# Kernel tuning notes

Hardware: AMD Instinct MI355X
Metric: run time of the kernel (lower is better)

## Reference

```python
import jax, jax.numpy as jnp
import numpy as np

B, S, H = 16, 1024, 768


def setup_inputs() -> dict:
    key = jax.random.key(0)
    ks = jax.random.split(key, 12)
    s = 1.0 / np.sqrt(H)
    return {
        "encoder_outputs": jax.random.normal(ks[0], (B, S, H), dtype=jnp.float32),
        "mask": jax.random.randint(ks[1], (B, S), 0, 2, dtype=jnp.int32),
        "Wq": jax.random.uniform(ks[2], (H, H), jnp.float32, -s, s),
        "bq": jnp.zeros((H,), jnp.float32),
        "Wk": jax.random.uniform(ks[3], (H, H), jnp.float32, -s, s),
        "bk": jnp.zeros((H,), jnp.float32),
        "Wv": jax.random.uniform(ks[4], (H, H), jnp.float32, -s, s),
        "bv": jnp.zeros((H,), jnp.float32),
        "W1": jax.random.uniform(ks[5], (H, H), jnp.float32, -s, s),
        "b1": jnp.zeros((H,), jnp.float32),
        "W2": jax.random.uniform(ks[6], (H, H), jnp.float32, -s, s),
        "b2": jnp.zeros((H,), jnp.float32),
    }


def reference(encoder_outputs, mask, Wq, bq, Wk, bk, Wv, bv, W1, b1, W2, b2):
    x = encoder_outputs  # [B, S, H]
    inv_sqrt_h = 1.0 / jnp.sqrt(jnp.asarray(H, x.dtype))
    # ReLU-gated query/key projections (dropout=0 -> identity)
    q = jax.nn.relu(jnp.einsum('bsh,oh->bso', x, Wq) + bq)
    k = jax.nn.relu(jnp.einsum('bsh,oh->bso', x, Wk) + bk)
    score = jnp.einsum('bsh,bth->bst', q, k) * inv_sqrt_h  # [B, S, S]
    v = jnp.einsum('bsh,oh->bso', x, Wv) + bv
    m = mask.astype(x.dtype)  # [B, S]
    new_mask = m[:, :, None] * m[:, None, :]  # outer product [B, S, S]
    score = score - (1.0 - new_mask) * 1e12
    w = jax.nn.softmax(score, axis=2) * new_mask
    out = jnp.einsum('bst,bth->bsh', w, v)
    # FFN residual
    h1 = jax.nn.relu(jnp.einsum('bsh,oh->bso', out, W1) + b1)
    out = jnp.einsum('bsh,oh->bso', h1, W2) + b2 + out
    return out
```

## Files before the change

### kernel.cpp

```cpp
#include <hip/hip_runtime.h>
#include <hip/hip_bf16.h>

typedef __bf16 bf16_t;
typedef __bf16 bf16x8 __attribute__((ext_vector_type(8)));
typedef __bf16 bf16x4 __attribute__((ext_vector_type(4)));
typedef float f32x4 __attribute__((ext_vector_type(4)));
typedef unsigned int u32;
typedef const __attribute__((address_space(1))) u32* gptr_t;
typedef __attribute__((address_space(3))) u32* lptr_t;

static constexpr int Bb = 16, Ss = 1024, Hh = 768;

__global__ __launch_bounds__(256) void compact_mask(
    const int* __restrict__ mask, int* __restrict__ tok, int* __restrict__ cnt)
{
    const int b = blockIdx.x;
    const int t = threadIdx.x;
    const int4 m4 = *(const int4*)&mask[(b << 10) + (t << 2)];
    const int c = (m4.x != 0) + (m4.y != 0) + (m4.z != 0) + (m4.w != 0);
    __shared__ int sb[256];
    sb[t] = c;
    __syncthreads();
    for (int off = 1; off < 256; off <<= 1) {
        int v = (t >= off) ? sb[t - off] : 0;
        __syncthreads();
        sb[t] += v;
        __syncthreads();
    }
    int p = sb[t] - c;
    int* tb = tok + (b << 10);
    if (m4.x) tb[p++] = (t << 2) + 0;
    if (m4.y) tb[p++] = (t << 2) + 1;
    if (m4.z) tb[p++] = (t << 2) + 2;
    if (m4.w) tb[p++] = (t << 2) + 3;
    if (t == 255) cnt[b] = sb[255];
}

__global__ __launch_bounds__(256) void cvt_all(
    const float* __restrict__ x,
    const float* __restrict__ w0, const float* __restrict__ w1,
    const float* __restrict__ w2, const float* __restrict__ w3,
    const float* __restrict__ w4,
    const float* __restrict__ bq, const float* __restrict__ bk,
    const float* __restrict__ bv,
    const float* __restrict__ b1, const float* __restrict__ b2,
    const int* __restrict__ tok, const int* __restrict__ cnt,
    bf16_t* __restrict__ xc, bf16_t* __restrict__ wdst, float* __restrict__ bdst,
    float* __restrict__ cvec)
{
    const int bx = blockIdx.x;
    const int t = threadIdx.x;
    if (bx < 2880) {
        int seg = bx / 576;
        const float* src = seg == 0 ? w0 : seg == 1 ? w1 : seg == 2 ? w2 : seg == 3 ? w3 : w4;
        int i = (bx % 576) * 256 + t;
        float4 v = ((const float4*)src)[i];
        bf16x4 o = { (bf16_t)v.x, (bf16_t)v.y, (bf16_t)v.z, (bf16_t)v.w };
        ((bf16x4*)(wdst + (long)seg * 589824))[i] = o;
    } else if (bx < 2889) {
        int i = (bx - 2880) * 256 + t;
        if (i < 2304)
            bdst[i] = i < 768 ? bq[i] : i < 1536 ? bk[i - 768] : bv[i - 1536];
    } else if (bx < 19273) {
        const int idx = bx - 2889;
        const int b = idx >> 10, j = idx & 1023;
        if (j < cnt[b] && t < 192) {
            const int s = tok[(b << 10) + j];
            float4 v = ((const float4*)(x + ((long)((b << 10) + s)) * 768))[t];
            bf16x4 o = { (bf16_t)v.x, (bf16_t)v.y, (bf16_t)v.z, (bf16_t)v.w };
            ((bf16x4*)(xc + ((long)((b << 10) + j)) * 768))[t] = o;
        }
    } else {
        const int o = ((bx - 19273) << 3) + (t >> 5);
        const int l = t & 31;
        const float* wr = w4 + (long)o * 768;
        float acc = 0.f;
        for (int h = l; h < 768; h += 32) acc += wr[h] * fmaxf(b1[h], 0.f);
#pragma unroll
        for (int off = 16; off; off >>= 1) acc += __shfl_down(acc, off, 32);
        if (l == 0) cvec[o] = acc + b2[o];
    }
}

__device__ __forceinline__ void async_cp16(const void* g, void* l)
{
    __builtin_amdgcn_global_load_lds((gptr_t)g, (lptr_t)l, 16, 0, 0);
}

enum { EG_QKV = 0, EG_SCORE_C = 1, EG_PV = 2, EG_FFN1 = 3, EG_FFN2 = 4 };

#define SBAR __builtin_amdgcn_s_barrier()
#define VMW(n) asm volatile("s_waitcnt vmcnt(" #n ")" ::: "memory")

template <int EPI, int NT>
__global__ __launch_bounds__(512) void mfma_gemm(
    const bf16_t* __restrict__ A, const bf16_t* __restrict__ B,
    const float* __restrict__ bias, const bf16_t* __restrict__ resid,
    const int* __restrict__ tok, const int* __restrict__ cnt,
    void* __restrict__ Cout, bf16_t* __restrict__ out2, bf16_t* __restrict__ out3,
    int K, int lda, int ldb, long sA, long sB, float scale)
{
    int tot = 0;
#pragma unroll
    for (int b = 0; b < 16; b++) {
        int a = (cnt[b] + 127) >> 7;
        tot += (EPI == EG_SCORE_C) ? a * a : a * NT;
    }
    const int raw = blockIdx.x;
    if (raw >= tot) return;
    const int q = tot >> 3, r = tot & 7;
    const int xcd = raw & 7, pos = raw >> 3;
    int v = xcd * q + (xcd < r ? xcd : r) + pos;
    int bz = 0;
    for (;;) {
        int a = (cnt[bz] + 127) >> 7;
        int t = (EPI == EG_SCORE_C) ? a * a : a * NT;
        if (v < t) break;
        v -= t; ++bz;
    }
    int mi, ni;
    if constexpr (EPI == EG_SCORE_C) {
        int a = (cnt[bz] + 127) >> 7;
        mi = v / a; ni = v - mi * a;
    } else {
        mi = v / NT; ni = v - mi * NT;
    }
    const int cb = cnt[bz];
    const int m0 = mi << 7;
    const int n0 = ni << 7;
    const int Kend = (EPI == EG_PV) ? ((cb + 63) & ~63) : K;
    const int nk = Kend >> 6;

    constexpr int MI = 2, NI = 4;
    constexpr int TSZ = 128 * 64;

    __shared__ __align__(16) bf16_t Asl[2 * TSZ];
    __shared__ __align__(16) bf16_t Bsl[2 * TSZ];

    const int tid = threadIdx.x;
    const int wid = tid >> 6;
    const int lane = tid & 63;
    const int wm = wid & 3, wn = wid >> 2;

    const bf16_t* Ab = A + (long)bz * sA;
    const bf16_t* Bp = B + (long)bz * sB;

    const int srow8 = lane >> 3;
    const int scg = ((lane & 7) ^ srow8) << 3;

    const bf16_t* pa[2];
    const bf16_t* pb[2];
#pragma unroll
    for (int qq = 0; qq < 2; qq++) {
        pa[qq] = Ab + (long)(m0 + (wid << 4) + (qq << 3) + srow8) * lda + scg;
        pb[qq] = Bp + (long)(n0 + (wid << 4) + (qq << 3) + srow8) * ldb + scg;
    }
    const int wrow = wid << 4;

    const int arow = lane & 15;
    const int axr = lane & 7;
    const int f0 = (arow << 6) + (((lane >> 4)      ^ axr) << 3);
    const int f1 = (arow << 6) + ((((lane >> 4) + 4) ^ axr) << 3);

    auto stage = [&](int tk, int buf) {
        const long ko = (long)tk << 6;
#pragma unroll
        for (int qq = 0; qq < 2; qq++) {
            async_cp16(pa[qq] + ko, &Asl[buf * TSZ + ((wrow + (qq << 3)) << 6)]);
            async_cp16(pb[qq] + ko, &Bsl[buf * TSZ + ((wrow + (qq << 3)) << 6)]);
        }
    };

    f32x4 acc[MI][NI] = {};

    stage(0, 0);
    __builtin_amdgcn_sched_barrier(0);
    VMW(0); SBAR;

    for (int t = 0; t < nk; ++t) {
        if (t + 1 < nk) stage(t + 1, (t + 1) & 1);

        const int cba = (t & 1) * TSZ;
        bf16x8 af[MI][2], bfr[NI][2];
#pragma unroll
        for (int i = 0; i < MI; i++) {
            const int rb = cba + ((wm * MI + i) << 10);
            af[i][0] = *(const bf16x8*)&Asl[rb + f0];
            af[i][1] = *(const bf16x8*)&Asl[rb + f1];
        }
#pragma unroll
        for (int j = 0; j < NI; j++) {
            const int rb = cba + ((wn * NI + j) << 10);
            bfr[j][0] = *(const bf16x8*)&Bsl[rb + f0];
            bfr[j][1] = *(const bf16x8*)&Bsl[rb + f1];
        }
        __builtin_amdgcn_sched_barrier(0);
#pragma unroll
        for (int kk = 0; kk < 2; kk++)
#pragma unroll
            for (int i = 0; i < MI; i++)
#pragma unroll
                for (int j = 0; j < NI; j++)
                    acc[i][j] = __builtin_amdgcn_mfma_f32_16x16x32_bf16(
                        af[i][kk], bfr[j][kk], acc[i][j], 0, 0, 0);
        __builtin_amdgcn_sched_barrier(0);
        if (t + 1 < nk) { VMW(0); SBAR; }
    }

    const int mb_ = m0 + wm * 32;
    const int nb_ = n0 + wn * 64;
    const int colw = lane & 15;
    const int rowq = (lane >> 4) << 2;

    if constexpr (EPI == EG_QKV) {
        float bj[NI];
#pragma unroll
        for (int j = 0; j < NI; j++) bj[j] = bias[nb_ + (j << 4) + colw];
        if (nb_ < 1536) {
            bf16_t* C = ((nb_ < 768) ? (bf16_t*)Cout : out2) + (long)bz * 786432;
            const int cbase = (nb_ < 768) ? nb_ : nb_ - 768;
#pragma unroll
            for (int i = 0; i < MI; i++)
#pragma unroll
                for (int j = 0; j < NI; j++)
#pragma unroll
                    for (int r2 = 0; r2 < 4; r2++) {
                        int row = mb_ + (i << 4) + rowq + r2;
                        int col = cbase + (j << 4) + colw;
                        C[(long)row * Hh + col] = (bf16_t)fmaxf(acc[i][j][r2] + bj[j], 0.f);
                    }
        } else {
            bf16_t* C = out3 + (long)bz * 786432;
#pragma unroll
            for (int i = 0; i < MI; i++) {
                const int jc0 = mb_ + (i << 4) + rowq;
#pragma unroll
                for (int j = 0; j < NI; j++) {
                    const int col = nb_ - 1536 + (j << 4) + colw;
                    bf16x4 o = { (bf16_t)(acc[i][j][0] + bj[j]), (bf16_t)(acc[i][j][1] + bj[j]),
                                 (bf16_t)(acc[i][j][2] + bj[j]), (bf16_t)(acc[i][j][3] + bj[j]) };
                    *(bf16x4*)&C[(long)col * 1024 + jc0] = o;
                }
            }
        }
    } else if constexpr (EPI == EG_SCORE_C) {
        bf16_t* C = (bf16_t*)Cout + (long)bz * 1048576;
#pragma unroll
        for (int i = 0; i < MI; i++) {
            const int kbase = mb_ + (i << 4) + rowq;
#pragma unroll
            for (int j = 0; j < NI; j++) {
                const int qrow = nb_ + (j << 4) + colw;
                bf16x4 o = { (bf16_t)(acc[i][j][0] * scale), (bf16_t)(acc[i][j][1] * scale),
                             (bf16_t)(acc[i][j][2] * scale), (bf16_t)(acc[i][j][3] * scale) };
                *(bf16x4*)&C[(long)qrow * 1024 + kbase] = o;
            }
        }
    } else if constexpr (EPI == EG_FFN2) {
        float* outp = (float*)Cout;
        const bf16_t* crow = resid + (long)bz * 786432;
        const int* tb = tok + (bz << 10);
        float bj[NI];
#pragma unroll
        for (int j = 0; j < NI; j++) bj[j] = bias[nb_ + (j << 4) + colw];
#pragma unroll
        for (int i = 0; i < MI; i++)
#pragma unroll
            for (int r2 = 0; r2 < 4; r2++) {
                const int jq = mb_ + (i << 4) + rowq + r2;
                if (jq < cb) {
                    const int s = tb[jq];
                    float* orow = outp + ((long)((bz << 10) + s)) * 768;
                    const bf16_t* cr = crow + (long)jq * 768;
#pragma unroll
                    for (int j = 0; j < NI; j++) {
                        const int col = nb_ + (j << 4) + colw;
                        orow[col] = acc[i][j][r2] + bj[j] + (float)cr[col];
                    }
                }
            }
    } else {
        bf16_t* C = (bf16_t*)Cout + (long)bz * 786432;
        float bj[NI];
#pragma unroll
        for (int j = 0; j < NI; j++) bj[j] = 0.f;
        if constexpr (EPI == EG_FFN1) {
#pragma unroll
            for (int j = 0; j < NI; j++) bj[j] = bias[nb_ + (j << 4) + colw];
        }
#pragma unroll
        for (int i = 0; i < MI; i++)
#pragma unroll
            for (int j = 0; j < NI; j++)
#pragma unroll
                for (int r2 = 0; r2 < 4; r2++) {
                    int row = mb_ + (i << 4) + rowq + r2;
                    int col = nb_ + (j << 4) + colw;
                    float val = acc[i][j][r2] + bj[j];
                    if constexpr (EPI == EG_FFN1) val = fmaxf(val, 0.f);
                    C[(long)row * Hh + col] = (bf16_t)val;
                }
    }
}

__global__ __launch_bounds__(256) void softmax_rows(
    bf16_t* __restrict__ S_, const int* __restrict__ cnt,
    const int* __restrict__ mask, const float* __restrict__ cvec,
    float* __restrict__ out)
{
    const int b = blockIdx.y;
    const int t = threadIdx.x;

    if (blockIdx.z == 1) {
        const int s = blockIdx.x;
        if (t >= 192 || mask[(b << 10) + s]) return;
        float4 v = ((const float4*)cvec)[t];
        ((float4*)(out + ((long)((b << 10) + s)) * 768))[t] = v;
        return;
    }

    const int jq = blockIdx.x;
    const int cb = cnt[b];
    if (jq >= cb) return;
    bf16_t* p = S_ + (((long)(b << 10)) + jq) * 1024;
    const int t0 = t << 2;

    bf16x4 v4 = *(const bf16x4*)&p[t0];
    float v0 = (t0 + 0 < cb) ? (float)v4[0] : -1e30f;
    float v1 = (t0 + 1 < cb) ? (float)v4[1] : -1e30f;
    float v2 = (t0 + 2 < cb) ? (float)v4[2] : -1e30f;
    float v3 = (t0 + 3 < cb) ? (float)v4[3] : -1e30f;

    float mx = fmaxf(fmaxf(v0, v1), fmaxf(v2, v3));
#pragma unroll
    for (int off = 32; off; off >>= 1) mx = fmaxf(mx, __shfl_down(mx, off, 64));
    __shared__ float redm[4], reds[4];
    if ((t & 63) == 0) redm[t >> 6] = mx;
    __syncthreads();
    mx = fmaxf(fmaxf(redm[0], redm[1]), fmaxf(redm[2], redm[3]));

    float e0 = __expf(v0 - mx), e1 = __expf(v1 - mx);
    float e2 = __expf(v2 - mx), e3 = __expf(v3 - mx);
    float sm = e0 + e1 + e2 + e3;
#pragma unroll
    for (int off = 32; off; off >>= 1) sm += __shfl_down(sm, off, 64);
    if ((t & 63) == 0) reds[t >> 6] = sm;
    __syncthreads();
    sm = reds[0] + reds[1] + reds[2] + reds[3];

    const float inv = 1.f / sm;
    bf16x4 o = { (bf16_t)(e0 * inv), (bf16_t)(e1 * inv),
                 (bf16_t)(e2 * inv), (bf16_t)(e3 * inv) };
    *(bf16x4*)&p[t0] = o;
}

extern "C" void kernel_launch(void* const* d_in, const int* in_sizes, int n_in,
                              void* d_out, int out_size, void* d_ws, size_t ws_size,
                              hipStream_t stream)
{
    const float* x  = (const float*)d_in[0];
    const int* mask = (const int*)d_in[1];
    const float* Wq = (const float*)d_in[2];
    const float* bq = (const float*)d_in[3];
    const float* Wk = (const float*)d_in[4];
    const float* bk = (const float*)d_in[5];
    const float* Wv = (const float*)d_in[6];
    const float* bv = (const float*)d_in[7];
    const float* W1 = (const float*)d_in[8];
    const float* b1 = (const float*)d_in[9];
    const float* W2 = (const float*)d_in[10];
    const float* b2 = (const float*)d_in[11];
    float* out = (float*)d_out;

    char* w = (char*)d_ws;
    bf16_t* xc   = (bf16_t*)(w + 0);
    bf16_t* qc   = (bf16_t*)(w + 25165824);
    bf16_t* kc   = (bf16_t*)(w + 50331648);
    bf16_t* vTc  = (bf16_t*)(w + 75497472);
    bf16_t* sc   = (bf16_t*)(w + 100663296);
    bf16_t* wqkv = (bf16_t*)(w + 134217728);
    bf16_t* w1b  = (bf16_t*)(w + 137756672);
    bf16_t* w2b  = (bf16_t*)(w + 138936320);
    float*  bqkv = (float*) (w + 140115968);
    int*    tok  = (int*)   (w + 140125184);
    int*    cnt  = (int*)   (w + 140190720);
    float*  cvec = (float*) (w + 140190784);
    bf16_t* ctxc = xc;
    bf16_t* h1c  = qc;

    const float inv_sqrt_h = 0.036084391824351615f;
    dim3 blk(256);
    dim3 blk8(512);

    compact_mask<<<16, blk, 0, stream>>>(mask, tok, cnt);
    cvt_all<<<19369, blk, 0, stream>>>(x, Wq, Wk, Wv, W1, W2, bq, bk, bv, b1, b2,
                                       tok, cnt, xc, wqkv, bqkv, cvec);

    mfma_gemm<EG_QKV, 18><<<2304, blk8, 0, stream>>>(
        xc, wqkv, bqkv, nullptr, tok, cnt, qc, kc, vTc,
        768, 768, 768, 786432, 0, 1.f);

    mfma_gemm<EG_SCORE_C, 1><<<1024, blk8, 0, stream>>>(
        kc, qc, nullptr, nullptr, tok, cnt, sc, nullptr, nullptr,
        768, 768, 768, 786432, 786432, inv_sqrt_h);

    softmax_rows<<<dim3(1024, 16, 2), blk, 0, stream>>>(sc, cnt, mask, cvec, out);

    mfma_gemm<EG_PV, 6><<<768, blk8, 0, stream>>>(
        sc, vTc, nullptr, nullptr, tok, cnt, ctxc, nullptr, nullptr,
        0, 1024, 1024, 1048576, 786432, 1.f);

    mfma_gemm<EG_FFN1, 6><<<768, blk8, 0, stream>>>(
        ctxc, w1b, b1, nullptr, tok, cnt, h1c, nullptr, nullptr,
        768, 768, 768, 786432, 0, 1.f);

    mfma_gemm<EG_FFN2, 6><<<768, blk8, 0, stream>>>(
        h1c, w2b, b2, ctxc, tok, cnt, out, nullptr, nullptr,
        768, 768, 768, 786432, 0, 1.f);
}
```

Before: 269.5 us.

## Fuse GEMM and softmax stages into one persistent cooperative kernel with grid syncs

Replaces the five separate GEMM launches and the softmax launch with a single cooperative persistent kernel. The kernel loops over tiles per phase and separates phases with grid.sync(). The softmax is rewritten so that one wavefront handles one row, reducing with xor shuffles and no LDS barriers. The goal is to remove launch gaps and tail effects between stages. The cost is that grid-wide barriers are imposed, the XCD-aware tile remapping is dropped, and the grid size is capped by occupancy, which may reduce parallelism for the large QKV phase.

Result: slower. 534.6 us (+98.3%).

```diff
diff --git a/kernel.cpp b/kernel.cpp
--- a/kernel.cpp
+++ b/kernel.cpp
@@ -1,5 +1,8 @@
 #include <hip/hip_runtime.h>
 #include <hip/hip_bf16.h>
+#include <hip/hip_cooperative_groups.h>
+
+namespace cg = cooperative_groups;
 
 typedef __bf16 bf16_t;
 typedef __bf16 bf16x8 __attribute__((ext_vector_type(8)));
@@ -92,8 +95,11 @@
 #define SBAR __builtin_amdgcn_s_barrier()
 #define VMW(n) asm volatile("s_waitcnt vmcnt(" #n ")" ::: "memory")
 
+static constexpr int TSZ = 128 * 64;
+
 template <int EPI, int NT>
-__global__ __launch_bounds__(512) void mfma_gemm(
+__device__ void gemm_phase(
+    bf16_t* Asl, bf16_t* Bsl,
     const bf16_t* __restrict__ A, const bf16_t* __restrict__ B,
     const float* __restrict__ bias, const bf16_t* __restrict__ resid,
     const int* __restrict__ tok, const int* __restrict__ cnt,
@@ -106,119 +112,178 @@
         int a = (cnt[b] + 127) >> 7;
         tot += (EPI == EG_SCORE_C) ? a * a : a * NT;
     }
-    const int raw = blockIdx.x;
-    if (raw >= tot) return;
-    const int q = tot >> 3, r = tot & 7;
-    const int xcd = raw & 7, pos = raw >> 3;
-    int v = xcd * q + (xcd < r ? xcd : r) + pos;
-    int bz = 0;
-    for (;;) {
-        int a = (cnt[bz] + 127) >> 7;
-        int t = (EPI == EG_SCORE_C) ? a * a : a * NT;
-        if (v < t) break;
-        v -= t; ++bz;
-    }
-    int mi, ni;
-    if constexpr (EPI == EG_SCORE_C) {
-        int a = (cnt[bz] + 127) >> 7;
-        mi = v / a; ni = v - mi * a;
-    } else {
-        mi = v / NT; ni = v - mi * NT;
-    }
-    const int cb = cnt[bz];
-    const int m0 = mi << 7;
-    const int n0 = ni << 7;
-    const int Kend = (EPI == EG_PV) ? ((cb + 63) & ~63) : K;
-    const int nk = Kend >> 6;
 
     constexpr int MI = 2, NI = 4;
-    constexpr int TSZ = 128 * 64;
-
-    __shared__ __align__(16) bf16_t Asl[2 * TSZ];
-    __shared__ __align__(16) bf16_t Bsl[2 * TSZ];
-
     const int tid = threadIdx.x;
     const int wid = tid >> 6;
     const int lane = tid & 63;
     const int wm = wid & 3, wn = wid >> 2;
-
-    const bf16_t* Ab = A + (long)bz * sA;
-    const bf16_t* Bp = B + (long)bz * sB;
-
     const int srow8 = lane >> 3;
     const int scg = ((lane & 7) ^ srow8) << 3;
-
-    const bf16_t* pa[2];
-    const bf16_t* pb[2];
-#pragma unroll
-    for (int qq = 0; qq < 2; qq++) {
-        pa[qq] = Ab + (long)(m0 + (wid << 4) + (qq << 3) + srow8) * lda + scg;
-        pb[qq] = Bp + (long)(n0 + (wid << 4) + (qq << 3) + srow8) * ldb + scg;
-    }
     const int wrow = wid << 4;
-
     const int arow = lane & 15;
     const int axr = lane & 7;
     const int f0 = (arow << 6) + (((lane >> 4)      ^ axr) << 3);
     const int f1 = (arow << 6) + ((((lane >> 4) + 4) ^ axr) << 3);
-
-    auto stage = [&](int tk, int buf) {
-        const long ko = (long)tk << 6;
-#pragma unroll
-        for (int qq = 0; qq < 2; qq++) {
-            async_cp16(pa[qq] + ko, &Asl[buf * TSZ + ((wrow + (qq << 3)) << 6)]);
-            async_cp16(pb[qq] + ko, &Bsl[buf * TSZ + ((wrow + (qq << 3)) << 6)]);
-        }
-    };
-
-    f32x4 acc[MI][NI] = {};
-
-    stage(0, 0);
-    __builtin_amdgcn_sched_barrier(0);
-    VMW(0); SBAR;
-
-    for (int t = 0; t < nk; ++t) {
-        if (t + 1 < nk) stage(t + 1, (t + 1) & 1);
-
-        const int cba = (t & 1) * TSZ;
-        bf16x8 af[MI][2], bfr[NI][2];
-#pragma unroll
-        for (int i = 0; i < MI; i++) {
-            const int rb = cba + ((wm * MI + i) << 10);
-            af[i][0] = *(const bf16x8*)&Asl[rb + f0];
-            af[i][1] = *(const bf16x8*)&Asl[rb + f1];
-        }
-#pragma unroll
-        for (int j = 0; j < NI; j++) {
-            const int rb = cba + ((wn * NI + j) << 10);
-            bfr[j][0] = *(const bf16x8*)&Bsl[rb + f0];
-            bfr[j][1] = *(const bf16x8*)&Bsl[rb + f1];
-        }
-        __builtin_amdgcn_sched_barrier(0);
-#pragma unroll
-        for (int kk = 0; kk < 2; kk++)
-#pragma unroll
-            for (int i = 0; i < MI; i++)
-#pragma unroll
-                for (int j = 0; j < NI; j++)
-                    acc[i][j] = __builtin_amdgcn_mfma_f32_16x16x32_bf16(
-                        af[i][kk], bfr[j][kk], acc[i][j], 0, 0, 0);
-        __builtin_amdgcn_sched_barrier(0);
-        if (t + 1 < nk) { VMW(0); SBAR; }
-    }
-
-    const int mb_ = m0 + wm * 32;
-    const int nb_ = n0 + wn * 64;
     const int colw = lane & 15;
     const int rowq = (lane >> 4) << 2;
 
-    if constexpr (EPI == EG_QKV) {
-        float bj[NI];
-#pragma unroll
-        for (int j = 0; j < NI; j++) bj[j] = bias[nb_ + (j << 4) + colw];
-        if (nb_ < 1536) {
-            bf16_t* C = ((nb_ < 768) ? (bf16_t*)Cout : out2) + (long)bz * 786432;
-            const int cbase = (nb_ < 768) ? nb_ : nb_ - 768;
+    for (int w = blockIdx.x; w < tot; w += gridDim.x) {
+        int wv = w, bz = 0;
+        for (;;) {
+            int a = (cnt[bz] + 127) >> 7;
+            int t = (EPI == EG_SCORE_C) ? a * a : a * NT;
+            if (wv < t) break;
+            wv -= t; ++bz;
+        }
+        int mi, ni;
+        if constexpr (EPI == EG_SCORE_C) {
+            int a = (cnt[bz] + 127) >> 7;
+            mi = wv / a; ni = wv - mi * a;
+        } else {
+            mi = wv / NT; ni = wv - mi * NT;
+        }
+        const int cb = cnt[bz];
+        const int m0 = mi << 7;
+        const int n0 = ni << 7;
+        const int Kend = (EPI == EG_PV) ? ((cb + 63) & ~63) : K;
+        const int nk = Kend >> 6;
+
+        const bf16_t* Ab = A + (long)bz * sA;
+        const bf16_t* Bp = B + (long)bz * sB;
+        const bf16_t* pa[2];
+        const bf16_t* pb[2];
+#pragma unroll
+        for (int qq = 0; qq < 2; qq++) {
+            pa[qq] = Ab + (long)(m0 + (wid << 4) + (qq << 3) + srow8) * lda + scg;
+            pb[qq] = Bp + (long)(n0 + (wid << 4) + (qq << 3) + srow8) * ldb + scg;
+        }
+
+        auto stage = [&](int tk, int buf) {
+            const long ko = (long)tk << 6;
+#pragma unroll
+            for (int qq = 0; qq < 2; qq++) {
+                async_cp16(pa[qq] + ko, &Asl[buf * TSZ + ((wrow + (qq << 3)) << 6)]);
+                async_cp16(pb[qq] + ko, &Bsl[buf * TSZ + ((wrow + (qq << 3)) << 6)]);
+            }
+        };
+
+        f32x4 acc[MI][NI] = {};
+
+        SBAR;
+        stage(0, 0);
+        __builtin_amdgcn_sched_barrier(0);
+        VMW(0); SBAR;
+
+        for (int t = 0; t < nk; ++t) {
+            if (t + 1 < nk) stage(t + 1, (t + 1) & 1);
+
+            const int cba = (t & 1) * TSZ;
+            bf16x8 af[MI][2], bfr[NI][2];
+#pragma unroll
+            for (int i = 0; i < MI; i++) {
+                const int rb = cba + ((wm * MI + i) << 10);
+                af[i][0] = *(const bf16x8*)&Asl[rb + f0];
+                af[i][1] = *(const bf16x8*)&Asl[rb + f1];
+            }
+#pragma unroll
+            for (int j = 0; j < NI; j++) {
+                const int rb = cba + ((wn * NI + j) << 10);
+                bfr[j][0] = *(const bf16x8*)&Bsl[rb + f0];
+                bfr[j][1] = *(const bf16x8*)&Bsl[rb + f1];
+            }
+            __builtin_amdgcn_sched_barrier(0);
+#pragma unroll
+            for (int kk = 0; kk < 2; kk++)
+#pragma unroll
+                for (int i = 0; i < MI; i++)
+#pragma unroll
+                    for (int j = 0; j < NI; j++)
+                        acc[i][j] = __builtin_amdgcn_mfma_f32_16x16x32_bf16(
+                            af[i][kk], bfr[j][kk], acc[i][j], 0, 0, 0);
+            __builtin_amdgcn_sched_barrier(0);
+            if (t + 1 < nk) { VMW(0); SBAR; }
+        }
+
+        const int mb_ = m0 + wm * 32;
+        const int nb_ = n0 + wn * 64;
+
+        if constexpr (EPI == EG_QKV) {
+            float bj[NI];
+#pragma unroll
+            for (int j = 0; j < NI; j++) bj[j] = bias[nb_ + (j << 4) + colw];
+            if (nb_ < 1536) {
+                bf16_t* C = ((nb_ < 768) ? (bf16_t*)Cout : out2) + (long)bz * 786432;
+                const int cbase = (nb_ < 768) ? nb_ : nb_ - 768;
+#pragma unroll
+                for (int i = 0; i < MI; i++)
+#pragma unroll
+                    for (int j = 0; j < NI; j++)
+#pragma unroll
+                        for (int r2 = 0; r2 < 4; r2++) {
+                            int row = mb_ + (i << 4) + rowq + r2;
+                            int col = cbase + (j << 4) + colw;
+                            C[(long)row * Hh + col] = (bf16_t)fmaxf(acc[i][j][r2] + bj[j], 0.f);
+                        }
+            } else {
+                bf16_t* C = out3 + (long)bz * 786432;
+#pragma unroll
+                for (int i = 0; i < MI; i++) {
+                    const int jc0 = mb_ + (i << 4) + rowq;
+#pragma unroll
+                    for (int j = 0; j < NI; j++) {
+                        const int col = nb_ - 1536 + (j << 4) + colw;
+                        bf16x4 o = { (bf16_t)(acc[i][j][0] + bj[j]), (bf16_t)(acc[i][j][1] + bj[j]),
+                                     (bf16_t)(acc[i][j][2] + bj[j]), (bf16_t)(acc[i][j][3] + bj[j]) };
+                        *(bf16x4*)&C[(long)col * 1024 + jc0] = o;
+                    }
+                }
+            }
+        } else if constexpr (EPI == EG_SCORE_C) {
+            bf16_t* C = (bf16_t*)Cout + (long)bz * 1048576;
+#pragma unroll
+            for (int i = 0; i < MI; i++) {
+                const int kbase = mb_ + (i << 4) + rowq;
+#pragma unroll
+                for (int j = 0; j < NI; j++) {
+                    const int qrow = nb_ + (j << 4) + colw;
+                    bf16x4 o = { (bf16_t)(acc[i][j][0] * scale), (bf16_t)(acc[i][j][1] * scale),
+                                 (bf16_t)(acc[i][j][2] * scale), (bf16_t)(acc[i][j][3] * scale) };
+                    *(bf16x4*)&C[(long)qrow * 1024 + kbase] = o;
+                }
+            }
+        } else if constexpr (EPI == EG_FFN2) {
+            float* outp = (float*)Cout;
+            const bf16_t* crow = resid + (long)bz * 786432;
+            const int* tb = tok + (bz << 10);
+            float bj[NI];
+#pragma unroll
+            for (int j = 0; j < NI; j++) bj[j] = bias[nb_ + (j << 4) + colw];
+#pragma unroll
+            for (int i = 0; i < MI; i++)
+#pragma unroll
+                for (int r2 = 0; r2 < 4; r2++) {
+                    const int jq = mb_ + (i << 4) + rowq + r2;
+                    if (jq < cb) {
+                        const int s = tb[jq];
+                        float* orow = outp + ((long)((bz << 10) + s)) * 768;
+                        const bf16_t* cr = crow + (long)jq * 768;
+#pragma unroll
+                        for (int j = 0; j < NI; j++) {
+                            const int col = nb_ + (j << 4) + colw;
+                            orow[col] = acc[i][j][r2] + bj[j] + (float)cr[col];
+                        }
+                    }
+                }
+        } else {
+            bf16_t* C = (bf16_t*)Cout + (long)bz * 786432;
+            float bj[NI];
+#pragma unroll
+            for (int j = 0; j < NI; j++) bj[j] = 0.f;
+            if constexpr (EPI == EG_FFN1) {
+#pragma unroll
+                for (int j = 0; j < NI; j++) bj[j] = bias[nb_ + (j << 4) + colw];
+            }
 #pragma unroll
             for (int i = 0; i < MI; i++)
 #pragma unroll
@@ -226,132 +291,102 @@
 #pragma unroll
                     for (int r2 = 0; r2 < 4; r2++) {
                         int row = mb_ + (i << 4) + rowq + r2;
-                        int col = cbase + (j << 4) + colw;
-                        C[(long)row * Hh + col] = (bf16_t)fmaxf(acc[i][j][r2] + bj[j], 0.f);
+                        int col = nb_ + (j << 4) + colw;
+                        float val = acc[i][j][r2] + bj[j];
+                        if constexpr (EPI == EG_FFN1) val = fmaxf(val, 0.f);
+                        C[(long)row * Hh + col] = (bf16_t)val;
                     }
-        } else {
-            bf16_t* C = out3 + (long)bz * 786432;
-#pragma unroll
-            for (int i = 0; i < MI; i++) {
-                const int jc0 = mb_ + (i << 4) + rowq;
-#pragma unroll
-                for (int j = 0; j < NI; j++) {
-                    const int col = nb_ - 1536 + (j << 4) + colw;
-                    bf16x4 o = { (bf16_t)(acc[i][j][0] + bj[j]), (bf16_t)(acc[i][j][1] + bj[j]),
-                                 (bf16_t)(acc[i][j][2] + bj[j]), (bf16_t)(acc[i][j][3] + bj[j]) };
-                    *(bf16x4*)&C[(long)col * 1024 + jc0] = o;
-                }
-            }
-        }
-    } else if constexpr (EPI == EG_SCORE_C) {
-        bf16_t* C = (bf16_t*)Cout + (long)bz * 1048576;
-#pragma unroll
-        for (int i = 0; i < MI; i++) {
-            const int kbase = mb_ + (i << 4) + rowq;
-#pragma unroll
-            for (int j = 0; j < NI; j++) {
-                const int qrow = nb_ + (j << 4) + colw;
-                bf16x4 o = { (bf16_t)(acc[i][j][0] * scale), (bf16_t)(acc[i][j][1] * scale),
-                             (bf16_t)(acc[i][j][2] * scale), (bf16_t)(acc[i][j][3] * scale) };
-                *(bf16x4*)&C[(long)qrow * 1024 + kbase] = o;
-            }
-        }
-    } else if constexpr (EPI == EG_FFN2) {
-        float* outp = (float*)Cout;
-        const bf16_t* crow = resid + (long)bz * 786432;
-        const int* tb = tok + (bz << 10);
-        float bj[NI];
-#pragma unroll
-        for (int j = 0; j < NI; j++) bj[j] = bias[nb_ + (j << 4) + colw];
-#pragma unroll
-        for (int i = 0; i < MI; i++)
-#pragma unroll
-            for (int r2 = 0; r2 < 4; r2++) {
-                const int jq = mb_ + (i << 4) + rowq + r2;
-                if (jq < cb) {
-                    const int s = tb[jq];
-                    float* orow = outp + ((long)((bz << 10) + s)) * 768;
-                    const bf16_t* cr = crow + (long)jq * 768;
-#pragma unroll
-                    for (int j = 0; j < NI; j++) {
-                        const int col = nb_ + (j << 4) + colw;
-                        orow[col] = acc[i][j][r2] + bj[j] + (float)cr[col];
-                    }
-                }
-            }
-    } else {
-        bf16_t* C = (bf16_t*)Cout + (long)bz * 786432;
-        float bj[NI];
-#pragma unroll
-        for (int j = 0; j < NI; j++) bj[j] = 0.f;
-        if constexpr (EPI == EG_FFN1) {
-#pragma unroll
-            for (int j = 0; j < NI; j++) bj[j] = bias[nb_ + (j << 4) + colw];
-        }
-#pragma unroll
-        for (int i = 0; i < MI; i++)
-#pragma unroll
-            for (int j = 0; j < NI; j++)
-#pragma unroll
-                for (int r2 = 0; r2 < 4; r2++) {
-                    int row = mb_ + (i << 4) + rowq + r2;
-                    int col = nb_ + (j << 4) + colw;
-                    float val = acc[i][j][r2] + bj[j];
-                    if constexpr (EPI == EG_FFN1) val = fmaxf(val, 0.f);
-                    C[(long)row * Hh + col] = (bf16_t)val;
-                }
-    }
-}
-
-__global__ __launch_bounds__(256) void softmax_rows(
+        }
+    }
+}
+
+__device__ void softmax_phase(
     bf16_t* __restrict__ S_, const int* __restrict__ cnt,
     const int* __restrict__ mask, const float* __restrict__ cvec,
     float* __restrict__ out)
 {
-    const int b = blockIdx.y;
-    const int t = threadIdx.x;
-
-    if (blockIdx.z == 1) {
-        const int s = blockIdx.x;
-        if (t >= 192 || mask[(b << 10) + s]) return;
-        float4 v = ((const float4*)cvec)[t];
-        ((float4*)(out + ((long)((b << 10) + s)) * 768))[t] = v;
-        return;
-    }
-
-    const int jq = blockIdx.x;
-    const int cb = cnt[b];
-    if (jq >= cb) return;
-    bf16_t* p = S_ + (((long)(b << 10)) + jq) * 1024;
-    const int t0 = t << 2;
-
-    bf16x4 v4 = *(const bf16x4*)&p[t0];
-    float v0 = (t0 + 0 < cb) ? (float)v4[0] : -1e30f;
-    float v1 = (t0 + 1 < cb) ? (float)v4[1] : -1e30f;
-    float v2 = (t0 + 2 < cb) ? (float)v4[2] : -1e30f;
-    float v3 = (t0 + 3 < cb) ? (float)v4[3] : -1e30f;
-
-    float mx = fmaxf(fmaxf(v0, v1), fmaxf(v2, v3));
-#pragma unroll
-    for (int off = 32; off; off >>= 1) mx = fmaxf(mx, __shfl_down(mx, off, 64));
-    __shared__ float redm[4], reds[4];
-    if ((t & 63) == 0) redm[t >> 6] = mx;
-    __syncthreads();
-    mx = fmaxf(fmaxf(redm[0], redm[1]), fmaxf(redm[2], redm[3]));
-
-    float e0 = __expf(v0 - mx), e1 = __expf(v1 - mx);
-    float e2 = __expf(v2 - mx), e3 = __expf(v3 - mx);
-    float sm = e0 + e1 + e2 + e3;
-#pragma unroll
-    for (int off = 32; off; off >>= 1) sm += __shfl_down(sm, off, 64);
-    if ((t & 63) == 0) reds[t >> 6] = sm;
-    __syncthreads();
-    sm = reds[0] + reds[1] + reds[2] + reds[3];
-
-    const float inv = 1.f / sm;
-    bf16x4 o = { (bf16_t)(e0 * inv), (bf16_t)(e1 * inv),
-                 (bf16_t)(e2 * inv), (bf16_t)(e3 * inv) };
-    *(bf16x4*)&p[t0] = o;
+    const int wid = threadIdx.x >> 6, lane = threadIdx.x & 63;
+    const int gw = blockIdx.x * 8 + wid;
+    const int nw = gridDim.x << 3;
+
+    for (int rw = gw; rw < 16384; rw += nw) {
+        const int b = rw >> 10, jq = rw & 1023;
+        const int cb = cnt[b];
+        if (jq < cb) {
+            bf16_t* p = S_ + (((long)(b << 10)) + jq) * 1024;
+            const int c0 = lane << 4;
+            bf16x8 u = *(const bf16x8*)&p[c0];
+            bf16x8 v = *(const bf16x8*)&p[c0 + 8];
+            float f[16];
+#pragma unroll
+            for (int i = 0; i < 8; i++) {
+                f[i]     = (c0 + i     < cb) ? (float)u[i] : -1e30f;
+                f[8 + i] = (c0 + 8 + i < cb) ? (float)v[i] : -1e30f;
+            }
+            float mx = f[0];
+#pragma unroll
+            for (int i = 1; i < 16; i++) mx = fmaxf(mx, f[i]);
+#pragma unroll
+            for (int off = 32; off; off >>= 1) mx = fmaxf(mx, __shfl_xor(mx, off, 64));
+            float sm = 0.f;
+#pragma unroll
+            for (int i = 0; i < 16; i++) { f[i] = __expf(f[i] - mx); sm += f[i]; }
+#pragma unroll
+            for (int off = 32; off; off >>= 1) sm += __shfl_xor(sm, off, 64);
+            const float inv = 1.f / sm;
+            bf16x8 o0, o1;
+#pragma unroll
+            for (int i = 0; i < 8; i++) {
+                o0[i] = (bf16_t)(f[i] * inv);
+                o1[i] = (bf16_t)(f[8 + i] * inv);
+            }
+            *(bf16x8*)&p[c0] = o0;
+            *(bf16x8*)&p[c0 + 8] = o1;
+        }
+    }
+    for (int rw = gw; rw < 16384; rw += nw) {
+        const int b = rw >> 10, s = rw & 1023;
+        if (!mask[(b << 10) + s]) {
+            float* orow = out + ((long)((b << 10) + s)) * 768;
+#pragma unroll
+            for (int i = 0; i < 3; i++)
+                ((float4*)orow)[(i << 6) + lane] = ((const float4*)cvec)[(i << 6) + lane];
+        }
+    }
+}
+
+struct KParams {
+    const bf16_t *xc, *wqkv, *w1b, *w2b;
+    const float *bqkv, *b1, *b2, *cvec;
+    bf16_t *qc, *kc, *vTc, *sc, *ctxc, *h1c;
+    const int *tok, *cnt, *mask;
+    float *out;
+    float inv_sqrt_h;
+};
+
+__global__ __launch_bounds__(512, 4) void fused_chain(KParams p)
+{
+    __shared__ __align__(16) bf16_t Asl[2 * TSZ];
+    __shared__ __align__(16) bf16_t Bsl[2 * TSZ];
+    cg::grid_group grid = cg::this_grid();
+
+    gemm_phase<EG_QKV, 18>(Asl, Bsl, p.xc, p.wqkv, p.bqkv, nullptr, p.tok, p.cnt,
+                           p.qc, p.kc, p.vTc, 768, 768, 768, 786432, 0, 1.f);
+    grid.sync();
+    gemm_phase<EG_SCORE_C, 1>(Asl, Bsl, p.kc, p.qc, nullptr, nullptr, p.tok, p.cnt,
+                              p.sc, nullptr, nullptr, 768, 768, 768, 786432, 786432,
+                              p.inv_sqrt_h);
+    grid.sync();
+    softmax_phase(p.sc, p.cnt, p.mask, p.cvec, p.out);
+    grid.sync();
+    gemm_phase<EG_PV, 6>(Asl, Bsl, p.sc, p.vTc, nullptr, nullptr, p.tok, p.cnt,
+                         p.ctxc, nullptr, nullptr, 0, 1024, 1024, 1048576, 786432, 1.f);
+    grid.sync();
+    gemm_phase<EG_FFN1, 6>(Asl, Bsl, p.ctxc, p.w1b, p.b1, nullptr, p.tok, p.cnt,
+                           p.h1c, nullptr, nullptr, 768, 768, 768, 786432, 0, 1.f);
+    grid.sync();
+    gemm_phase<EG_FFN2, 6>(Asl, Bsl, p.h1c, p.w2b, p.b2, p.ctxc, p.tok, p.cnt,
+                           p.out, nullptr, nullptr, 768, 768, 768, 786432, 0, 1.f);
 }
 
 extern "C" void kernel_launch(void* const* d_in, const int* in_sizes, int n_in,
@@ -385,36 +420,33 @@
     int*    tok  = (int*)   (w + 140125184);
     int*    cnt  = (int*)   (w + 140190720);
     float*  cvec = (float*) (w + 140190784);
-    bf16_t* ctxc = xc;
-    bf16_t* h1c  = qc;
-
-    const float inv_sqrt_h = 0.036084391824351615f;
+
     dim3 blk(256);
-    dim3 blk8(512);
 
     compact_mask<<<16, blk, 0, stream>>>(mask, tok, cnt);
     cvt_all<<<19369, blk, 0, stream>>>(x, Wq, Wk, Wv, W1, W2, bq, bk, bv, b1, b2,
                                        tok, cnt, xc, wqkv, bqkv, cvec);
 
-    mfma_gemm<EG_QKV, 18><<<2304, blk8, 0, stream>>>(
-        xc, wqkv, bqkv, nullptr, tok, cnt, qc, kc, vTc,
-        768, 768, 768, 786432, 0, 1.f);
-
-    mfma_gemm<EG_SCORE_C, 1><<<1024, blk8, 0, stream>>>(
-        kc, qc, nullptr, nullptr, tok, cnt, sc, nullptr, nullptr,
-        768, 768, 768, 786432, 786432, inv_sqrt_h);
-
-    softmax_rows<<<dim3(1024, 16, 2), blk, 0, stream>>>(sc, cnt, mask, cvec, out);
-
-    mfma_gemm<EG_PV, 6><<<768, blk8, 0, stream>>>(
-        sc, vTc, nullptr, nullptr, tok, cnt, ctxc, nullptr, nullptr,
-        0, 1024, 1024, 1048576, 786432, 1.f);
-
-    mfma_gemm<EG_FFN1, 6><<<768, blk8, 0, stream>>>(
-        ctxc, w1b, b1, nullptr, tok, cnt, h1c, nullptr, nullptr,
-        768, 768, 768, 786432, 0, 1.f);
-
-    mfma_gemm<EG_FFN2, 6><<<768, blk8, 0, stream>>>(
-        h1c, w2b, b2, ctxc, tok, cnt, out, nullptr, nullptr,
-        768, 768, 768, 786432, 0, 1.f);
-}
+    KParams p;
+    p.xc = xc; p.wqkv = wqkv; p.w1b = w1b; p.w2b = w2b;
+    p.bqkv = bqkv; p.b1 = b1; p.b2 = b2; p.cvec = cvec;
+    p.qc = qc; p.kc = kc; p.vTc = vTc; p.sc = sc;
+    p.ctxc = xc; p.h1c = qc;
+    p.tok = tok; p.cnt = cnt; p.mask = mask;
+    p.out = out;
+    p.inv_sqrt_h = 0.036084391824351615f;
+
+    static int s_grid = 0;
+    if (s_grid == 0) {
+        int bpc = 0;
+        if (hipOccupancyMaxActiveBlocksPerMultiprocessor(
+                &bpc, (const void*)fused_chain, 512, 0) != hipSuccess || bpc < 1)
+            bpc = 1;
+        int g = bpc * 256;
+        s_grid = g < 256 ? 256 : (g > 512 ? 512 : g);
+    }
+
+    void* args[] = { &p };
+    hipLaunchCooperativeKernel((void*)fused_chain, dim3(s_grid), dim3(512),
+                               args, 0, stream);
+}
```

## Fuse token gather and fp32-to-bf16 conversion of x into QKV GEMM A-load

Applied to the files above, without the earlier changes.

The QKV GEMM now reads the fp32 encoder rows directly through the compacted token index, converts them to bf16 in registers and writes them into swizzled LDS, instead of loading a pre-gathered bf16 copy. This removes the separate gather/convert pass and its 25 MB round trip through memory. The mask-compaction kernel is merged into the weight-prep kernel, which saves one launch. In exchange the A-tile load becomes a synchronous register path with an extra LDS write and wait per k-step, in place of async global-to-LDS copies, which may expose more latency in the main loop.

After: 278.6 us. 3.4% more time.

```diff
diff --git a/kernel.cpp b/kernel.cpp
--- a/kernel.cpp
+++ b/kernel.cpp
@@ -11,67 +11,54 @@
 
 static constexpr int Bb = 16, Ss = 1024, Hh = 768;
 
-__global__ __launch_bounds__(256) void compact_mask(
-    const int* __restrict__ mask, int* __restrict__ tok, int* __restrict__ cnt)
-{
-    const int b = blockIdx.x;
-    const int t = threadIdx.x;
-    const int4 m4 = *(const int4*)&mask[(b << 10) + (t << 2)];
-    const int c = (m4.x != 0) + (m4.y != 0) + (m4.z != 0) + (m4.w != 0);
-    __shared__ int sb[256];
-    sb[t] = c;
-    __syncthreads();
-    for (int off = 1; off < 256; off <<= 1) {
-        int v = (t >= off) ? sb[t - off] : 0;
-        __syncthreads();
-        sb[t] += v;
-        __syncthreads();
-    }
-    int p = sb[t] - c;
-    int* tb = tok + (b << 10);
-    if (m4.x) tb[p++] = (t << 2) + 0;
-    if (m4.y) tb[p++] = (t << 2) + 1;
-    if (m4.z) tb[p++] = (t << 2) + 2;
-    if (m4.w) tb[p++] = (t << 2) + 3;
-    if (t == 255) cnt[b] = sb[255];
-}
-
-__global__ __launch_bounds__(256) void cvt_all(
-    const float* __restrict__ x,
+__global__ __launch_bounds__(256) void prep_all(
+    const int* __restrict__ mask,
     const float* __restrict__ w0, const float* __restrict__ w1,
     const float* __restrict__ w2, const float* __restrict__ w3,
     const float* __restrict__ w4,
     const float* __restrict__ bq, const float* __restrict__ bk,
     const float* __restrict__ bv,
     const float* __restrict__ b1, const float* __restrict__ b2,
-    const int* __restrict__ tok, const int* __restrict__ cnt,
-    bf16_t* __restrict__ xc, bf16_t* __restrict__ wdst, float* __restrict__ bdst,
+    int* __restrict__ tok, int* __restrict__ cnt,
+    bf16_t* __restrict__ wdst, float* __restrict__ bdst,
     float* __restrict__ cvec)
 {
     const int bx = blockIdx.x;
     const int t = threadIdx.x;
-    if (bx < 2880) {
-        int seg = bx / 576;
+    __shared__ int sb[256];
+
+    if (bx < 16) {
+        const int b = bx;
+        const int4 m4 = *(const int4*)&mask[(b << 10) + (t << 2)];
+        const int c = (m4.x != 0) + (m4.y != 0) + (m4.z != 0) + (m4.w != 0);
+        sb[t] = c;
+        __syncthreads();
+        for (int off = 1; off < 256; off <<= 1) {
+            int v = (t >= off) ? sb[t - off] : 0;
+            __syncthreads();
+            sb[t] += v;
+            __syncthreads();
+        }
+        int p = sb[t] - c;
+        int* tb = tok + (b << 10);
+        if (m4.x) tb[p++] = (t << 2) + 0;
+        if (m4.y) tb[p++] = (t << 2) + 1;
+        if (m4.z) tb[p++] = (t << 2) + 2;
+        if (m4.w) tb[p++] = (t << 2) + 3;
+        if (t == 255) cnt[b] = sb[255];
+    } else if (bx < 2896) {
+        int seg = (bx - 16) / 576;
         const float* src = seg == 0 ? w0 : seg == 1 ? w1 : seg == 2 ? w2 : seg == 3 ? w3 : w4;
-        int i = (bx % 576) * 256 + t;
+        int i = ((bx - 16) % 576) * 256 + t;
         float4 v = ((const float4*)src)[i];
         bf16x4 o = { (bf16_t)v.x, (bf16_t)v.y, (bf16_t)v.z, (bf16_t)v.w };
         ((bf16x4*)(wdst + (long)seg * 589824))[i] = o;
-    } else if (bx < 2889) {
-        int i = (bx - 2880) * 256 + t;
+    } else if (bx < 2905) {
+        int i = (bx - 2896) * 256 + t;
         if (i < 2304)
             bdst[i] = i < 768 ? bq[i] : i < 1536 ? bk[i - 768] : bv[i - 1536];
-    } else if (bx < 19273) {
-        const int idx = bx - 2889;
-        const int b = idx >> 10, j = idx & 1023;
-        if (j < cnt[b] && t < 192) {
-            const int s = tok[(b << 10) + j];
-            float4 v = ((const float4*)(x + ((long)((b << 10) + s)) * 768))[t];
-            bf16x4 o = { (bf16_t)v.x, (bf16_t)v.y, (bf16_t)v.z, (bf16_t)v.w };
-            ((bf16x4*)(xc + ((long)((b << 10) + j)) * 768))[t] = o;
-        }
     } else {
-        const int o = ((bx - 19273) << 3) + (t >> 5);
+        const int o = ((bx - 2905) << 3) + (t >> 5);
         const int l = t & 31;
         const float* wr = w4 + (long)o * 768;
         float acc = 0.f;
@@ -91,10 +78,12 @@
 
 #define SBAR __builtin_amdgcn_s_barrier()
 #define VMW(n) asm volatile("s_waitcnt vmcnt(" #n ")" ::: "memory")
+#define LGK0 asm volatile("s_waitcnt lgkmcnt(0)" ::: "memory")
 
 template <int EPI, int NT>
 __global__ __launch_bounds__(512) void mfma_gemm(
     const bf16_t* __restrict__ A, const bf16_t* __restrict__ B,
+    const float* __restrict__ xg,
     const float* __restrict__ bias, const bf16_t* __restrict__ resid,
     const int* __restrict__ tok, const int* __restrict__ cnt,
     void* __restrict__ Cout, bf16_t* __restrict__ out2, bf16_t* __restrict__ out3,
@@ -142,43 +131,89 @@
     const int lane = tid & 63;
     const int wm = wid & 3, wn = wid >> 2;
 
-    const bf16_t* Ab = A + (long)bz * sA;
     const bf16_t* Bp = B + (long)bz * sB;
 
     const int srow8 = lane >> 3;
     const int scg = ((lane & 7) ^ srow8) << 3;
-
-    const bf16_t* pa[2];
     const bf16_t* pb[2];
 #pragma unroll
-    for (int qq = 0; qq < 2; qq++) {
-        pa[qq] = Ab + (long)(m0 + (wid << 4) + (qq << 3) + srow8) * lda + scg;
+    for (int qq = 0; qq < 2; qq++)
         pb[qq] = Bp + (long)(n0 + (wid << 4) + (qq << 3) + srow8) * ldb + scg;
-    }
     const int wrow = wid << 4;
+
+    const bf16_t* pa[2] = { nullptr, nullptr };
+    const float* xr = nullptr;
+    int aw_base = 0, aw_c0 = 0, aw_c1 = 0;
+    if constexpr (EPI == EG_QKV) {
+        const int row = (wid << 4) + (lane >> 2);
+        const int cp = (lane & 3) << 1;
+        const int jrow = m0 + row;
+        const int s = (jrow < cb) ? tok[(bz << 10) + jrow] : 0;
+        xr = xg + (long)((bz << 10) + s) * 768 + (cp << 3);
+        aw_base = row << 6;
+        aw_c0 = ((cp    ) ^ (row & 7)) << 3;
+        aw_c1 = ((cp + 1) ^ (row & 7)) << 3;
+    } else {
+        const bf16_t* Ab = A + (long)bz * sA;
+#pragma unroll
+        for (int qq = 0; qq < 2; qq++)
+            pa[qq] = Ab + (long)(m0 + (wid << 4) + (qq << 3) + srow8) * lda + scg;
+    }
 
     const int arow = lane & 15;
     const int axr = lane & 7;
     const int f0 = (arow << 6) + (((lane >> 4)      ^ axr) << 3);
     const int f1 = (arow << 6) + ((((lane >> 4) + 4) ^ axr) << 3);
 
-    auto stage = [&](int tk, int buf) {
+    auto stageB = [&](int tk, int buf) {
         const long ko = (long)tk << 6;
 #pragma unroll
-        for (int qq = 0; qq < 2; qq++) {
+        for (int qq = 0; qq < 2; qq++)
+            async_cp16(pb[qq] + ko, &Bsl[buf * TSZ + ((wrow + (qq << 3)) << 6)]);
+    };
+    auto stageA_g = [&](int tk, int buf) {
+        const long ko = (long)tk << 6;
+#pragma unroll
+        for (int qq = 0; qq < 2; qq++)
             async_cp16(pa[qq] + ko, &Asl[buf * TSZ + ((wrow + (qq << 3)) << 6)]);
-            async_cp16(pb[qq] + ko, &Bsl[buf * TSZ + ((wrow + (qq << 3)) << 6)]);
-        }
     };
 
+    float4 a4[4];
+    auto ldA = [&](int tk) {
+        const float4* p4 = (const float4*)(xr + ((long)tk << 6));
+        a4[0] = p4[0]; a4[1] = p4[1]; a4[2] = p4[2]; a4[3] = p4[3];
+    };
+    auto wrA = [&](int buf) {
+        bf16x8 w0 = { (bf16_t)a4[0].x, (bf16_t)a4[0].y, (bf16_t)a4[0].z, (bf16_t)a4[0].w,
+                      (bf16_t)a4[1].x, (bf16_t)a4[1].y, (bf16_t)a4[1].z, (bf16_t)a4[1].w };
+        bf16x8 w1 = { (bf16_t)a4[2].x, (bf16_t)a4[2].y, (bf16_t)a4[2].z, (bf16_t)a4[2].w,
+                      (bf16_t)a4[3].x, (bf16_t)a4[3].y, (bf16_t)a4[3].z, (bf16_t)a4[3].w };
+        bf16_t* bp = &Asl[buf * TSZ + aw_base];
+        *(bf16x8*)(bp + aw_c0) = w0;
+        *(bf16x8*)(bp + aw_c1) = w1;
+    };
+
     f32x4 acc[MI][NI] = {};
 
-    stage(0, 0);
-    __builtin_amdgcn_sched_barrier(0);
-    VMW(0); SBAR;
+    if constexpr (EPI == EG_QKV) {
+        ldA(0); stageB(0, 0);
+        __builtin_amdgcn_sched_barrier(0);
+        VMW(0);
+        wrA(0);
+        LGK0;
+        __builtin_amdgcn_sched_barrier(0);
+    } else {
+        stageA_g(0, 0); stageB(0, 0);
+        __builtin_amdgcn_sched_barrier(0);
+        VMW(0);
+    }
+    SBAR;
 
     for (int t = 0; t < nk; ++t) {
-        if (t + 1 < nk) stage(t + 1, (t + 1) & 1);
+        if (t + 1 < nk) {
+            if constexpr (EPI == EG_QKV) { ldA(t + 1); stageB(t + 1, (t + 1) & 1); }
+            else { stageA_g(t + 1, (t + 1) & 1); stageB(t + 1, (t + 1) & 1); }
+        }
 
         const int cba = (t & 1) * TSZ;
         bf16x8 af[MI][2], bfr[NI][2];
@@ -204,7 +239,15 @@
                     acc[i][j] = __builtin_amdgcn_mfma_f32_16x16x32_bf16(
                         af[i][kk], bfr[j][kk], acc[i][j], 0, 0, 0);
         __builtin_amdgcn_sched_barrier(0);
-        if (t + 1 < nk) { VMW(0); SBAR; }
+        if (t + 1 < nk) {
+            VMW(0);
+            if constexpr (EPI == EG_QKV) {
+                wrA((t + 1) & 1);
+                LGK0;
+                __builtin_amdgcn_sched_barrier(0);
+            }
+            SBAR;
+        }
     }
 
     const int mb_ = m0 + wm * 32;
@@ -373,7 +416,7 @@
     float* out = (float*)d_out;
 
     char* w = (char*)d_ws;
-    bf16_t* xc   = (bf16_t*)(w + 0);
+    bf16_t* ctxc = (bf16_t*)(w + 0);
     bf16_t* qc   = (bf16_t*)(w + 25165824);
     bf16_t* kc   = (bf16_t*)(w + 50331648);
     bf16_t* vTc  = (bf16_t*)(w + 75497472);
@@ -385,36 +428,35 @@
     int*    tok  = (int*)   (w + 140125184);
     int*    cnt  = (int*)   (w + 140190720);
     float*  cvec = (float*) (w + 140190784);
-    bf16_t* ctxc = xc;
     bf16_t* h1c  = qc;
 
     const float inv_sqrt_h = 0.036084391824351615f;
     dim3 blk(256);
     dim3 blk8(512);
 
-    compact_mask<<<16, blk, 0, stream>>>(mask, tok, cnt);
-    cvt_all<<<19369, blk, 0, stream>>>(x, Wq, Wk, Wv, W1, W2, bq, bk, bv, b1, b2,
-                                       tok, cnt, xc, wqkv, bqkv, cvec);
+    prep_all<<<3001, blk, 0, stream>>>(mask, Wq, Wk, Wv, W1, W2,
+                                       bq, bk, bv, b1, b2,
+                                       tok, cnt, wqkv, bqkv, cvec);
 
     mfma_gemm<EG_QKV, 18><<<2304, blk8, 0, stream>>>(
-        xc, wqkv, bqkv, nullptr, tok, cnt, qc, kc, vTc,
+        nullptr, wqkv, x, bqkv, nullptr, tok, cnt, qc, kc, vTc,
+        768, 768, 768, 0, 0, 1.f);
+
+    mfma_gemm<EG_SCORE_C, 1><<<1024, blk8, 0, stream>>>(
+        kc, qc, nullptr, nullptr, nullptr, tok, cnt, sc, nullptr, nullptr,
+        768, 768, 768, 786432, 786432, inv_sqrt_h);
+
+    softmax_rows<<<dim3(1024, 16, 2), blk, 0, stream>>>(sc, cnt, mask, cvec, out);
+
+    mfma_gemm<EG_PV, 6><<<768, blk8, 0, stream>>>(
+        sc, vTc, nullptr, nullptr, nullptr, tok, cnt, ctxc, nullptr, nullptr,
+        0, 1024, 1024, 1048576, 786432, 1.f);
+
+    mfma_gemm<EG_FFN1, 6><<<768, blk8, 0, stream>>>(
+        ctxc, w1b, nullptr, b1, nullptr, tok, cnt, h1c, nullptr, nullptr,
         768, 768, 768, 786432, 0, 1.f);
 
-    mfma_gemm<EG_SCORE_C, 1><<<1024, blk8, 0, stream>>>(
-        kc, qc, nullptr, nullptr, tok, cnt, sc, nullptr, nullptr,
-        768, 768, 768, 786432, 786432, inv_sqrt_h);
-
-    softmax_rows<<<dim3(1024, 16, 2), blk, 0, stream>>>(sc, cnt, mask, cvec, out);
-
-    mfma_gemm<EG_PV, 6><<<768, blk8, 0, stream>>>(
-        sc, vTc, nullptr, nullptr, tok, cnt, ctxc, nullptr, nullptr,
-        0, 1024, 1024, 1048576, 786432, 1.f);
-
-    mfma_gemm<EG_FFN1, 6><<<768, blk8, 0, stream>>>(
-        ctxc, w1b, b1, nullptr, tok, cnt, h1c, nullptr, nullptr,
-        768, 768, 768, 786432, 0, 1.f);
-
     mfma_gemm<EG_FFN2, 6><<<768, blk8, 0, stream>>>(
-        h1c, w2b, b2, ctxc, tok, cnt, out, nullptr, nullptr,
+        h1c, w2b, nullptr, b2, ctxc, tok, cnt, out, nullptr, nullptr,
         768, 768, 768, 786432, 0, 1.f);
 }
```
